# Kernel tuning notes

Hardware: AMD Instinct MI355X
Metric: run time of the kernel (lower is better)

The kernel has to match this reference:

```python
import jax, jax.numpy as jnp
import numpy as np

V, I, H, O = 10000, 64, 128, 128   # vocab, in_size, hidden_size, out_size
T, L = 4096, 64                    # num traces, max trace length


def setup_inputs() -> dict:
    key = jax.random.key(0)
    ks = jax.random.split(key, 18)
    s = 0.05
    n = jax.random.normal
    inp = {
        "emb":   n(ks[0], (V, I)) * s,
        # torch nn.LSTM layer 0: weight_ih [4H, I], weight_hh [4H, H], biases [4H]
        "W_ih1": n(ks[1], (4 * H, I)) * s,
        "W_hh1": n(ks[2], (4 * H, H)) * s,
        "b_ih1": n(ks[3], (4 * H,)) * s,
        "b_hh1": n(ks[4], (4 * H,)) * s,
        # layer 1
        "W_ih2": n(ks[5], (4 * H, H)) * s,
        "W_hh2": n(ks[6], (4 * H, H)) * s,
        "b_ih2": n(ks[7], (4 * H,)) * s,
        "b_hh2": n(ks[8], (4 * H,)) * s,
        # attention MLP: hidden -> 64 -> 1
        "Wp1":   n(ks[9], (64, H)) * s,
        "bp1":   n(ks[10], (64,)) * s,
        "Wp2":   n(ks[11], (1, 64)) * s,
        "bp2":   n(ks[12], (1,)) * s,
        # out_layer
        "W_out": n(ks[13], (O, H)) * s,
        "b_out": n(ks[14], (O,)) * s,
        "traces": jax.random.randint(ks[15], (T, L), 0, V, dtype=jnp.int32),
        "lengths": jnp.maximum(jax.random.randint(ks[16], (T,), 1, L + 1, dtype=jnp.int32), 1),
    }
    return inp


def _lstm_step(x, W_ih, b_ih, b_hh):
    # Single LSTM timestep from zero state (h0=c0=0), per token.
    # Gate order in torch: i, f, g, o. f*c0 = 0 so f is computed-but-unused.
    g = x @ W_ih.T + b_ih + b_hh                      # [T, L, 4H]
    i, f, c_hat, o = jnp.split(g, 4, axis=-1)
    c = jax.nn.sigmoid(i) * jnp.tanh(c_hat)
    return jax.nn.sigmoid(o) * jnp.tanh(c)            # [T, L, H]


def reference(emb, W_ih1, W_hh1, b_ih1, b_hh1, W_ih2, W_hh2, b_ih2, b_hh2,
              Wp1, bp1, Wp2, bp2, W_out, b_out, traces, lengths):
    x = emb[traces]                                   # [T, L, I]
    h1 = _lstm_step(x, W_ih1, b_ih1, b_hh1)           # [T, L, H]
    h2 = _lstm_step(h1, W_ih2, b_ih2, b_hh2)          # [T, L, H]  (hidden_out)
    # SelfAttention over positions within each trace
    energy = (jax.nn.relu(h2 @ Wp1.T + bp1) @ Wp2.T + bp2)[..., 0]  # [T, L]
    mask = jnp.arange(L)[None, :] < lengths[:, None]  # [T, L] valid positions
    energy = jnp.where(mask, energy, -1e30)
    w = jax.nn.softmax(energy, axis=1)                # [T, L]
    trace_emb = jnp.einsum("tlh,tl->th", h2, w)      # [T, H]
    final = trace_emb.sum(axis=0)                     # [H]  (sum over traces)
    return final @ W_out.T + b_out                    # [O]
```

## Files before the change

kernel.cpp:

```cpp
#include <hip/hip_runtime.h>
#include <stdint.h>

typedef unsigned short u16;
typedef __attribute__((ext_vector_type(8))) short short8;
typedef __attribute__((ext_vector_type(4))) float f32x4;
typedef __attribute__((ext_vector_type(4))) unsigned int u32x4;

#define NTRACE 4096
#define TLEN   64
#define ISZ    64
#define HSZ    128
#define NBIN   64
#define VSZ    10000

#define LOG2E     1.44269504088896f
#define TWOLOG2E  2.88539008177793f

__device__ __forceinline__ float bflo(uint32_t u) {
  union { uint32_t i; float f; } v; v.i = u << 16; return v.f;
}
__device__ __forceinline__ float bfhi(uint32_t u) {
  union { uint32_t i; float f; } v; v.i = u & 0xffff0000u; return v.f;
}
__device__ __forceinline__ u16 f2bf(float f) {
  union { float f; uint32_t i; } v; v.f = f;
  uint32_t r = v.i + 0x7fffu + ((v.i >> 16) & 1u);
  return (u16)(r >> 16);
}
__device__ __forceinline__ float fexp2(float x) {
  float r;
  asm("v_exp_f32 %0, %1" : "=v"(r) : "v"(x));
  return r;
}
__device__ __forceinline__ float gate2(float gB, float gE) {
  float E = fexp2(gE);
  float B = fexp2(gB);
  return (E - 1.0f) * __builtin_amdgcn_rcpf((E + 1.0f) * (1.0f + B));
}
__device__ __forceinline__ short8 mk8(uint32_t a, uint32_t b, uint32_t c, uint32_t d) {
  union { short8 s; uint32_t u[4]; } z;
  z.u[0] = a; z.u[1] = b; z.u[2] = c; z.u[3] = d; return z.s;
}
union S8 { short8 s; u16 h[8]; };
__device__ __forceinline__ int perm128(int rr) {
  return ((rr >> 4) & 3) * 32 + ((rr >> 2) & 3) * 8 + ((rr >> 6) & 1) * 4 + (rr & 3);
}

__global__ __launch_bounds__(128, 2) void k_vocab(
    const float* __restrict__ emb,
    const float* __restrict__ W1, const float* __restrict__ W2,
    const float* __restrict__ b_ih1, const float* __restrict__ b_hh1,
    const float* __restrict__ b_ih2, const float* __restrict__ b_hh2,
    const float* __restrict__ Wp1,
    const float* __restrict__ bp1v, const float* __restrict__ wp2v,
    float* __restrict__ Et, u16* __restrict__ H2t,
    float* __restrict__ bins)
{
  __shared__ __align__(16) u16 w1s[384 * 64];
  __shared__ __align__(16) u16 w2s[384 * 128];
  __shared__ float bsh1[512];
  __shared__ float bsh2[512];
  const int tid = threadIdx.x;

  {
    const int i = blockIdx.x * 128 + tid;
    if (i < NBIN * HSZ) bins[i] = 0.f;
  }

  for (int i = tid; i < 3072; i += 128) {
    const int r   = i >> 3;
    const int G3  = r >> 7;
    const int rawG = (G3 == 0) ? 0 : ((G3 == 1) ? 2 : 3);
    const int src = rawG * 128 + perm128(r & 127);
    const float s = (G3 == 1) ? TWOLOG2E : -LOG2E;
    const int c16 = (i & 7) * 8;
    const float* wsrc = W1 + (size_t)src * ISZ + c16;
    uint32_t pkk[4];
#pragma unroll
    for (int k = 0; k < 4; ++k)
      pkk[k] = (uint32_t)f2bf(wsrc[2 * k] * s) |
               ((uint32_t)f2bf(wsrc[2 * k + 1] * s) << 16);
    *(u32x4*)&w1s[r * 64 + (c16 ^ ((r & 7) << 3))] = *(u32x4*)pkk;
  }
  for (int i = tid; i < 6144; i += 128) {
    const int r   = i >> 4;
    const int G3  = r >> 7;
    const int rawG = (G3 == 0) ? 0 : ((G3 == 1) ? 2 : 3);
    const int src = rawG * 128 + perm128(r & 127);
    const float s = (G3 == 1) ? TWOLOG2E : -LOG2E;
    const int c16 = (i & 15) * 8;
    const float* wsrc = W2 + (size_t)src * HSZ + c16;
    uint32_t pkk[4];
#pragma unroll
    for (int k = 0; k < 4; ++k)
      pkk[k] = (uint32_t)f2bf(wsrc[2 * k] * s) |
               ((uint32_t)f2bf(wsrc[2 * k + 1] * s) << 16);
    *(u32x4*)&w2s[r * 128 + (c16 ^ ((r & 15) << 3))] = *(u32x4*)pkk;
  }
  for (int i = tid; i < 512; i += 128) {
    const int G = i >> 7, rr = i & 127;
    const float s = (G == 2) ? TWOLOG2E : -LOG2E;
    const int src = G * 128 + perm128(rr);
    bsh1[i] = (b_ih1[src] + b_hh1[src]) * s;
    bsh2[i] = (b_ih2[src] + b_hh2[src]) * s;
  }
  __syncthreads();

  const int lane = tid & 63;
  const int col  = lane & 15;
  const int q    = lane >> 4;
  const int sw1  = (col & 7) << 3;
  const int sw2  = col << 3;
  const int wbase = (blockIdx.x * 2 + (tid >> 6)) * 32;
  const f32x4 z = {0.f, 0.f, 0.f, 0.f};

  short8 xf[2][2];
#pragma unroll
  for (int g = 0; g < 2; ++g) {
    const int id = wbase + g * 16 + col;
    const int idc = (id < VSZ) ? id : 0;
    const float* xr = emb + (size_t)idc * ISZ + q * 8;
#pragma unroll
    for (int ks = 0; ks < 2; ++ks) {
      S8 v;
#pragma unroll
      for (int k = 0; k < 8; ++k) v.h[k] = f2bf(xr[ks * 32 + k]);
      xf[g][ks] = v.s;
    }
  }

  uint32_t pk[2][8][2];
#pragma unroll
  for (int mt = 0; mt < 8; ++mt) {
    f32x4 aI[2], aC[2], aO[2];
#pragma unroll
    for (int g = 0; g < 2; ++g) { aI[g] = z; aC[g] = z; aO[g] = z; }
#pragma unroll
    for (int ks = 0; ks < 2; ++ks) {
      const int off = ((ks * 32 + q * 8) ^ sw1);
      short8 fI = *(const short8*)&w1s[(mt * 16 + col) * ISZ + off];
      short8 fC = *(const short8*)&w1s[(128 + mt * 16 + col) * ISZ + off];
      short8 fO = *(const short8*)&w1s[(256 + mt * 16 + col) * ISZ + off];
#pragma unroll
      for (int g = 0; g < 2; ++g) {
        aI[g] = __builtin_amdgcn_mfma_f32_16x16x32_bf16(fI, xf[g][ks], aI[g], 0, 0, 0);
        aC[g] = __builtin_amdgcn_mfma_f32_16x16x32_bf16(fC, xf[g][ks], aC[g], 0, 0, 0);
        aO[g] = __builtin_amdgcn_mfma_f32_16x16x32_bf16(fO, xf[g][ks], aO[g], 0, 0, 0);
      }
    }
    float bI[4], bC[4], bO[4];
#pragma unroll
    for (int r = 0; r < 4; ++r) {
      const int h = mt * 16 + q * 4 + r;
      bI[r] = bsh1[h]; bC[r] = bsh1[256 + h]; bO[r] = bsh1[384 + h];
    }
#pragma unroll
    for (int g = 0; g < 2; ++g) {
      u16 hv[4];
#pragma unroll
      for (int r = 0; r < 4; ++r) {
        float c = gate2(aI[g][r] + bI[r], aC[g][r] + bC[r]);
        hv[r] = f2bf(gate2(aO[g][r] + bO[r], TWOLOG2E * c));
      }
      pk[g][mt][0] = (uint32_t)hv[0] | ((uint32_t)hv[1] << 16);
      pk[g][mt][1] = (uint32_t)hv[2] | ((uint32_t)hv[3] << 16);
    }
  }

  short8 hf[2][4];
#pragma unroll
  for (int g = 0; g < 2; ++g)
#pragma unroll
    for (int ks = 0; ks < 4; ++ks)
      hf[g][ks] = mk8(pk[g][ks][0], pk[g][ks][1], pk[g][ks + 4][0], pk[g][ks + 4][1]);

  uint32_t pk2[2][8][2];
#pragma unroll
  for (int mt = 0; mt < 8; ++mt) {
    f32x4 aI[2], aC[2], aO[2];
#pragma unroll
    for (int g = 0; g < 2; ++g) { aI[g] = z; aC[g] = z; aO[g] = z; }
#pragma unroll
    for (int ks = 0; ks < 4; ++ks) {
      const int off = ((ks * 32 + q * 8) ^ sw2);
      short8 fI = *(const short8*)&w2s[(mt * 16 + col) * HSZ + off];
      short8 fC = *(const short8*)&w2s[(128 + mt * 16 + col) * HSZ + off];
      short8 fO = *(const short8*)&w2s[(256 + mt * 16 + col) * HSZ + off];
#pragma unroll
      for (int g = 0; g < 2; ++g) {
        aI[g] = __builtin_amdgcn_mfma_f32_16x16x32_bf16(fI, hf[g][ks], aI[g], 0, 0, 0);
        aC[g] = __builtin_amdgcn_mfma_f32_16x16x32_bf16(fC, hf[g][ks], aC[g], 0, 0, 0);
        aO[g] = __builtin_amdgcn_mfma_f32_16x16x32_bf16(fO, hf[g][ks], aO[g], 0, 0, 0);
      }
    }
    float bI[4], bC[4], bO[4];
#pragma unroll
    for (int r = 0; r < 4; ++r) {
      const int h = mt * 16 + q * 4 + r;
      bI[r] = bsh2[h]; bC[r] = bsh2[256 + h]; bO[r] = bsh2[384 + h];
    }
#pragma unroll
    for (int g = 0; g < 2; ++g) {
      u16 hv[4];
#pragma unroll
      for (int r = 0; r < 4; ++r) {
        float c = gate2(aI[g][r] + bI[r], aC[g][r] + bC[r]);
        hv[r] = f2bf(gate2(aO[g][r] + bO[r], TWOLOG2E * c));
      }
      pk2[g][mt][0] = (uint32_t)hv[0] | ((uint32_t)hv[1] << 16);
      pk2[g][mt][1] = (uint32_t)hv[2] | ((uint32_t)hv[3] << 16);
    }
  }

  short8 hf2[2][4];
#pragma unroll
  for (int g = 0; g < 2; ++g)
#pragma unroll
    for (int ks = 0; ks < 4; ++ks)
      hf2[g][ks] = mk8(pk2[g][ks][0], pk2[g][ks][1], pk2[g][ks + 4][0], pk2[g][ks + 4][1]);

  float ep[2];
#pragma unroll
  for (int g = 0; g < 2; ++g) ep[g] = 0.f;
#pragma unroll
  for (int mt = 0; mt < 4; ++mt) {
    f32x4 acc[2];
#pragma unroll
    for (int g = 0; g < 2; ++g) acc[g] = z;
#pragma unroll
    for (int ks = 0; ks < 4; ++ks) {
      const float* wr = Wp1 + (size_t)(mt * 16 + col) * HSZ + ks * 32 + q * 8;
      S8 v;
#pragma unroll
      for (int k = 0; k < 8; ++k) v.h[k] = f2bf(wr[k]);
      const short8 fA = v.s;
#pragma unroll
      for (int g = 0; g < 2; ++g)
        acc[g] = __builtin_amdgcn_mfma_f32_16x16x32_bf16(fA, hf2[g][ks], acc[g], 0, 0, 0);
    }
#pragma unroll
    for (int r = 0; r < 4; ++r) {
      const int hp = mt * 16 + q * 4 + r;
      const float b1 = bp1v[hp];
      const float w2 = wp2v[hp];
#pragma unroll
      for (int g = 0; g < 2; ++g)
        ep[g] += fmaxf(acc[g][r] + b1, 0.f) * w2;
    }
  }
#pragma unroll
  for (int g = 0; g < 2; ++g) {
    ep[g] += __shfl_xor(ep[g], 16);
    ep[g] += __shfl_xor(ep[g], 32);
  }

#pragma unroll
  for (int g = 0; g < 2; ++g) {
    const int id = wbase + g * 16 + col;
    if (id < VSZ) {
      if (q == 0) Et[id] = ep[g];
#pragma unroll
      for (int ks = 0; ks < 4; ++ks)
        *(short8*)&H2t[(size_t)id * HSZ + ks * 32 + q * 8] = hf2[g][ks];
    }
  }
}

__global__ __launch_bounds__(256) void k_attn(
    const float* __restrict__ Et, const u16* __restrict__ H2t,
    const int* __restrict__ traces, const int* __restrict__ lengths,
    float* __restrict__ bins)
{
  const int wv   = threadIdx.x >> 6;
  const int lane = threadIdx.x & 63;
  const int t    = blockIdx.x * 4 + wv;
  const int len  = lengths[t];
  const int tok  = traces[t * TLEN + lane];
  const bool valid = lane < len;

  float e = valid ? Et[tok] : -3.0e38f;
  float m = e;
#pragma unroll
  for (int off = 1; off < 64; off <<= 1) m = fmaxf(m, __shfl_xor(m, off));
  float w = valid ? __expf(e - m) : 0.f;
  float s = w;
#pragma unroll
  for (int off = 1; off < 64; off <<= 1) s += __shfl_xor(s, off);
  const float wl = w * __builtin_amdgcn_rcpf(s);

  const int hc = lane * 2;
  float a0 = 0.f, a1 = 0.f;
  for (int l = 0; l < len; ++l) {
    const float wb = __shfl(wl, l);
    const int   tb = __shfl(tok, l);
    const uint32_t hv = *(const uint32_t*)&H2t[(size_t)tb * HSZ + hc];
    a0 += wb * bflo(hv);
    a1 += wb * bfhi(hv);
  }
  float* bin = bins + (size_t)(t & (NBIN - 1)) * HSZ;
  atomicAdd(&bin[hc], a0);
  atomicAdd(&bin[hc + 1], a1);
}

__global__ __launch_bounds__(128) void k_out(
    const float* __restrict__ bins, const float* __restrict__ W_out,
    const float* __restrict__ b_out, float* __restrict__ out)
{
  const int o = threadIdx.x;
  __shared__ float fs[HSZ];
  float s = 0.f;
#pragma unroll 4
  for (int b = 0; b < NBIN; ++b) s += bins[b * HSZ + o];
  fs[o] = s;
  __syncthreads();
  float acc = b_out[o];
  const float* wr = W_out + (size_t)o * HSZ;
#pragma unroll
  for (int h = 0; h < HSZ; ++h) acc += wr[h] * fs[h];
  out[o] = acc;
}

extern "C" void kernel_launch(void* const* d_in, const int* in_sizes, int n_in,
                              void* d_out, int out_size, void* d_ws, size_t ws_size,
                              hipStream_t stream)
{
  const float* emb   = (const float*)d_in[0];
  const float* W_ih1 = (const float*)d_in[1];
  const float* b_ih1 = (const float*)d_in[3];
  const float* b_hh1 = (const float*)d_in[4];
  const float* W_ih2 = (const float*)d_in[5];
  const float* b_ih2 = (const float*)d_in[7];
  const float* b_hh2 = (const float*)d_in[8];
  const float* Wp1   = (const float*)d_in[9];
  const float* bp1   = (const float*)d_in[10];
  const float* Wp2   = (const float*)d_in[11];
  const float* bp2   = (const float*)d_in[12];
  const float* W_out = (const float*)d_in[13];
  const float* b_out = (const float*)d_in[14];
  const int* traces  = (const int*)d_in[15];
  const int* lengths = (const int*)d_in[16];
  (void)bp2;

  char* ws = (char*)d_ws;
  float* Et   = (float*)(ws);
  u16*   H2t  = (u16*)(ws + 40960);
  float* bins = (float*)(ws + 2662400);

  k_vocab<<<160, 128, 0, stream>>>(emb, W_ih1, W_ih2, b_ih1, b_hh1,
                                   b_ih2, b_hh2, Wp1, bp1, Wp2,
                                   Et, H2t, bins);
  k_attn<<<NTRACE / 4, 256, 0, stream>>>(Et, H2t, traces, lengths, bins);
  k_out<<<1, 128, 0, stream>>>(bins, W_out, b_out, (float*)d_out);
}
```

Measured before the change: 153.7 us.

## Split weight conversion into prep kernel and widen vocab blocks to 512 threads

Adds a k_prep kernel that converts and swizzles the LSTM and attention weights to bf16 once, writing them to workspace along with pre-scaled biases and zeroed bins. k_vocab then copies the prepacked weights straight into shared memory. It now runs 80 blocks of 512 threads, with each wave handling 16 vocab rows instead of 32. The aim is to stop every block from redoing the fp32-to-bf16 conversion and to spread the per-block weight load across more waves. The cost is one extra kernel launch and less MFMA operand reuse per wave, and the biases and Wp1 are now read from global memory rather than shared memory.

```diff
diff --git a/kernel.cpp b/kernel.cpp
--- a/kernel.cpp
+++ b/kernel.cpp
@@ -46,64 +46,73 @@
   return ((rr >> 4) & 3) * 32 + ((rr >> 2) & 3) * 8 + ((rr >> 6) & 1) * 4 + (rr & 3);
 }
 
-__global__ __launch_bounds__(128, 2) void k_vocab(
-    const float* __restrict__ emb,
+__global__ __launch_bounds__(256) void k_prep(
     const float* __restrict__ W1, const float* __restrict__ W2,
+    const float* __restrict__ Wp1,
     const float* __restrict__ b_ih1, const float* __restrict__ b_hh1,
     const float* __restrict__ b_ih2, const float* __restrict__ b_hh2,
-    const float* __restrict__ Wp1,
-    const float* __restrict__ bp1v, const float* __restrict__ wp2v,
-    float* __restrict__ Et, u16* __restrict__ H2t,
+    u16* __restrict__ w1c, u16* __restrict__ w2c, u16* __restrict__ wp1b,
+    float* __restrict__ bs1, float* __restrict__ bs2,
     float* __restrict__ bins)
 {
-  __shared__ __align__(16) u16 w1s[384 * 64];
-  __shared__ __align__(16) u16 w2s[384 * 128];
-  __shared__ float bsh1[512];
-  __shared__ float bsh2[512];
-  const int tid = threadIdx.x;
-
-  {
-    const int i = blockIdx.x * 128 + tid;
-    if (i < NBIN * HSZ) bins[i] = 0.f;
-  }
-
-  for (int i = tid; i < 3072; i += 128) {
-    const int r   = i >> 3;
-    const int G3  = r >> 7;
+  const int i = blockIdx.x * 256 + threadIdx.x;
+  if (i < 3072) {
+    const int r    = i >> 3;
+    const int G3   = r >> 7;
     const int rawG = (G3 == 0) ? 0 : ((G3 == 1) ? 2 : 3);
-    const int src = rawG * 128 + perm128(r & 127);
-    const float s = (G3 == 1) ? TWOLOG2E : -LOG2E;
-    const int c16 = (i & 7) * 8;
+    const int src  = rawG * 128 + perm128(r & 127);
+    const float s  = (G3 == 1) ? TWOLOG2E : -LOG2E;
+    const int c16  = (i & 7) * 8;
     const float* wsrc = W1 + (size_t)src * ISZ + c16;
     uint32_t pkk[4];
 #pragma unroll
     for (int k = 0; k < 4; ++k)
       pkk[k] = (uint32_t)f2bf(wsrc[2 * k] * s) |
                ((uint32_t)f2bf(wsrc[2 * k + 1] * s) << 16);
-    *(u32x4*)&w1s[r * 64 + (c16 ^ ((r & 7) << 3))] = *(u32x4*)pkk;
-  }
-  for (int i = tid; i < 6144; i += 128) {
-    const int r   = i >> 4;
-    const int G3  = r >> 7;
+    *(u32x4*)&w1c[r * 64 + (c16 ^ ((r & 7) << 3))] = *(u32x4*)pkk;
+  }
+  if (i < 6144) {
+    const int r    = i >> 4;
+    const int G3   = r >> 7;
     const int rawG = (G3 == 0) ? 0 : ((G3 == 1) ? 2 : 3);
-    const int src = rawG * 128 + perm128(r & 127);
-    const float s = (G3 == 1) ? TWOLOG2E : -LOG2E;
-    const int c16 = (i & 15) * 8;
+    const int src  = rawG * 128 + perm128(r & 127);
+    const float s  = (G3 == 1) ? TWOLOG2E : -LOG2E;
+    const int c16  = (i & 15) * 8;
     const float* wsrc = W2 + (size_t)src * HSZ + c16;
     uint32_t pkk[4];
 #pragma unroll
     for (int k = 0; k < 4; ++k)
       pkk[k] = (uint32_t)f2bf(wsrc[2 * k] * s) |
                ((uint32_t)f2bf(wsrc[2 * k + 1] * s) << 16);
-    *(u32x4*)&w2s[r * 128 + (c16 ^ ((r & 15) << 3))] = *(u32x4*)pkk;
-  }
-  for (int i = tid; i < 512; i += 128) {
+    *(u32x4*)&w2c[r * 128 + (c16 ^ ((r & 15) << 3))] = *(u32x4*)pkk;
+  }
+  if (i < 64 * 128) wp1b[i] = f2bf(Wp1[i]);
+  if (i < 512) {
     const int G = i >> 7, rr = i & 127;
     const float s = (G == 2) ? TWOLOG2E : -LOG2E;
     const int src = G * 128 + perm128(rr);
-    bsh1[i] = (b_ih1[src] + b_hh1[src]) * s;
-    bsh2[i] = (b_ih2[src] + b_hh2[src]) * s;
-  }
+    bs1[i] = (b_ih1[src] + b_hh1[src]) * s;
+    bs2[i] = (b_ih2[src] + b_hh2[src]) * s;
+  }
+  if (i < NBIN * HSZ) bins[i] = 0.f;
+}
+
+__global__ __launch_bounds__(512) void k_vocab(
+    const float* __restrict__ emb,
+    const u16* __restrict__ w1c, const u16* __restrict__ w2c,
+    const float* __restrict__ bs1, const float* __restrict__ bs2,
+    const u16* __restrict__ wp1b,
+    const float* __restrict__ bp1v, const float* __restrict__ wp2v,
+    float* __restrict__ Et, u16* __restrict__ H2t)
+{
+  __shared__ __align__(16) u16 w1s[384 * 64];
+  __shared__ __align__(16) u16 w2s[384 * 128];
+  const int tid = threadIdx.x;
+
+  for (int i = tid; i < 3072; i += 512)
+    ((u32x4*)w1s)[i] = ((const u32x4*)w1c)[i];
+  for (int i = tid; i < 6144; i += 512)
+    ((u32x4*)w2s)[i] = ((const u32x4*)w2c)[i];
   __syncthreads();
 
   const int lane = tid & 63;
@@ -111,158 +120,105 @@
   const int q    = lane >> 4;
   const int sw1  = (col & 7) << 3;
   const int sw2  = col << 3;
-  const int wbase = (blockIdx.x * 2 + (tid >> 6)) * 32;
+  const int id   = (blockIdx.x * 8 + (tid >> 6)) * 16 + col;
+  const int idc  = (id < VSZ) ? id : 0;
   const f32x4 z = {0.f, 0.f, 0.f, 0.f};
 
-  short8 xf[2][2];
-#pragma unroll
-  for (int g = 0; g < 2; ++g) {
-    const int id = wbase + g * 16 + col;
-    const int idc = (id < VSZ) ? id : 0;
+  short8 xf[2];
+  {
     const float* xr = emb + (size_t)idc * ISZ + q * 8;
 #pragma unroll
     for (int ks = 0; ks < 2; ++ks) {
       S8 v;
 #pragma unroll
       for (int k = 0; k < 8; ++k) v.h[k] = f2bf(xr[ks * 32 + k]);
-      xf[g][ks] = v.s;
-    }
-  }
-
-  uint32_t pk[2][8][2];
+      xf[ks] = v.s;
+    }
+  }
+
+  uint32_t pk[8][2];
 #pragma unroll
   for (int mt = 0; mt < 8; ++mt) {
-    f32x4 aI[2], aC[2], aO[2];
-#pragma unroll
-    for (int g = 0; g < 2; ++g) { aI[g] = z; aC[g] = z; aO[g] = z; }
+    f32x4 aI = z, aC = z, aO = z;
 #pragma unroll
     for (int ks = 0; ks < 2; ++ks) {
       const int off = ((ks * 32 + q * 8) ^ sw1);
       short8 fI = *(const short8*)&w1s[(mt * 16 + col) * ISZ + off];
       short8 fC = *(const short8*)&w1s[(128 + mt * 16 + col) * ISZ + off];
       short8 fO = *(const short8*)&w1s[(256 + mt * 16 + col) * ISZ + off];
-#pragma unroll
-      for (int g = 0; g < 2; ++g) {
-        aI[g] = __builtin_amdgcn_mfma_f32_16x16x32_bf16(fI, xf[g][ks], aI[g], 0, 0, 0);
-        aC[g] = __builtin_amdgcn_mfma_f32_16x16x32_bf16(fC, xf[g][ks], aC[g], 0, 0, 0);
-        aO[g] = __builtin_amdgcn_mfma_f32_16x16x32_bf16(fO, xf[g][ks], aO[g], 0, 0, 0);
-      }
-    }
-    float bI[4], bC[4], bO[4];
+      aI = __builtin_amdgcn_mfma_f32_16x16x32_bf16(fI, xf[ks], aI, 0, 0, 0);
+      aC = __builtin_amdgcn_mfma_f32_16x16x32_bf16(fC, xf[ks], aC, 0, 0, 0);
+      aO = __builtin_amdgcn_mfma_f32_16x16x32_bf16(fO, xf[ks], aO, 0, 0, 0);
+    }
+    u16 hv[4];
 #pragma unroll
     for (int r = 0; r < 4; ++r) {
       const int h = mt * 16 + q * 4 + r;
-      bI[r] = bsh1[h]; bC[r] = bsh1[256 + h]; bO[r] = bsh1[384 + h];
-    }
-#pragma unroll
-    for (int g = 0; g < 2; ++g) {
-      u16 hv[4];
-#pragma unroll
-      for (int r = 0; r < 4; ++r) {
-        float c = gate2(aI[g][r] + bI[r], aC[g][r] + bC[r]);
-        hv[r] = f2bf(gate2(aO[g][r] + bO[r], TWOLOG2E * c));
-      }
-      pk[g][mt][0] = (uint32_t)hv[0] | ((uint32_t)hv[1] << 16);
-      pk[g][mt][1] = (uint32_t)hv[2] | ((uint32_t)hv[3] << 16);
-    }
-  }
-
-  short8 hf[2][4];
-#pragma unroll
-  for (int g = 0; g < 2; ++g)
-#pragma unroll
-    for (int ks = 0; ks < 4; ++ks)
-      hf[g][ks] = mk8(pk[g][ks][0], pk[g][ks][1], pk[g][ks + 4][0], pk[g][ks + 4][1]);
-
-  uint32_t pk2[2][8][2];
+      float c = gate2(aI[r] + bs1[h], aC[r] + bs1[256 + h]);
+      hv[r] = f2bf(gate2(aO[r] + bs1[384 + h], TWOLOG2E * c));
+    }
+    pk[mt][0] = (uint32_t)hv[0] | ((uint32_t)hv[1] << 16);
+    pk[mt][1] = (uint32_t)hv[2] | ((uint32_t)hv[3] << 16);
+  }
+
+  short8 hf[4];
+#pragma unroll
+  for (int ks = 0; ks < 4; ++ks)
+    hf[ks] = mk8(pk[ks][0], pk[ks][1], pk[ks + 4][0], pk[ks + 4][1]);
+
+  uint32_t pk2[8][2];
 #pragma unroll
   for (int mt = 0; mt < 8; ++mt) {
-    f32x4 aI[2], aC[2], aO[2];
-#pragma unroll
-    for (int g = 0; g < 2; ++g) { aI[g] = z; aC[g] = z; aO[g] = z; }
+    f32x4 aI = z, aC = z, aO = z;
 #pragma unroll
     for (int ks = 0; ks < 4; ++ks) {
       const int off = ((ks * 32 + q * 8) ^ sw2);
       short8 fI = *(const short8*)&w2s[(mt * 16 + col) * HSZ + off];
       short8 fC = *(const short8*)&w2s[(128 + mt * 16 + col) * HSZ + off];
       short8 fO = *(const short8*)&w2s[(256 + mt * 16 + col) * HSZ + off];
-#pragma unroll
-      for (int g = 0; g < 2; ++g) {
-        aI[g] = __builtin_amdgcn_mfma_f32_16x16x32_bf16(fI, hf[g][ks], aI[g], 0, 0, 0);
-        aC[g] = __builtin_amdgcn_mfma_f32_16x16x32_bf16(fC, hf[g][ks], aC[g], 0, 0, 0);
-        aO[g] = __builtin_amdgcn_mfma_f32_16x16x32_bf16(fO, hf[g][ks], aO[g], 0, 0, 0);
-      }
-    }
-    float bI[4], bC[4], bO[4];
+      aI = __builtin_amdgcn_mfma_f32_16x16x32_bf16(fI, hf[ks], aI, 0, 0, 0);
+      aC = __builtin_amdgcn_mfma_f32_16x16x32_bf16(fC, hf[ks], aC, 0, 0, 0);
+      aO = __builtin_amdgcn_mfma_f32_16x16x32_bf16(fO, hf[ks], aO, 0, 0, 0);
+    }
+    u16 hv[4];
 #pragma unroll
     for (int r = 0; r < 4; ++r) {
       const int h = mt * 16 + q * 4 + r;
-      bI[r] = bsh2[h]; bC[r] = bsh2[256 + h]; bO[r] = bsh2[384 + h];
-    }
-#pragma unroll
-    for (int g = 0; g < 2; ++g) {
-      u16 hv[4];
-#pragma unroll
-      for (int r = 0; r < 4; ++r) {
-        float c = gate2(aI[g][r] + bI[r], aC[g][r] + bC[r]);
-        hv[r] = f2bf(gate2(aO[g][r] + bO[r], TWOLOG2E * c));
-      }
-      pk2[g][mt][0] = (uint32_t)hv[0] | ((uint32_t)hv[1] << 16);
-      pk2[g][mt][1] = (uint32_t)hv[2] | ((uint32_t)hv[3] << 16);
-    }
-  }
-
-  short8 hf2[2][4];
-#pragma unroll
-  for (int g = 0; g < 2; ++g)
-#pragma unroll
-    for (int ks = 0; ks < 4; ++ks)
-      hf2[g][ks] = mk8(pk2[g][ks][0], pk2[g][ks][1], pk2[g][ks + 4][0], pk2[g][ks + 4][1]);
-
-  float ep[2];
-#pragma unroll
-  for (int g = 0; g < 2; ++g) ep[g] = 0.f;
+      float c = gate2(aI[r] + bs2[h], aC[r] + bs2[256 + h]);
+      hv[r] = f2bf(gate2(aO[r] + bs2[384 + h], TWOLOG2E * c));
+    }
+    pk2[mt][0] = (uint32_t)hv[0] | ((uint32_t)hv[1] << 16);
+    pk2[mt][1] = (uint32_t)hv[2] | ((uint32_t)hv[3] << 16);
+  }
+
+  short8 hf2[4];
+#pragma unroll
+  for (int ks = 0; ks < 4; ++ks)
+    hf2[ks] = mk8(pk2[ks][0], pk2[ks][1], pk2[ks + 4][0], pk2[ks + 4][1]);
+
+  float ep = 0.f;
 #pragma unroll
   for (int mt = 0; mt < 4; ++mt) {
-    f32x4 acc[2];
-#pragma unroll
-    for (int g = 0; g < 2; ++g) acc[g] = z;
+    f32x4 acc = z;
 #pragma unroll
     for (int ks = 0; ks < 4; ++ks) {
-      const float* wr = Wp1 + (size_t)(mt * 16 + col) * HSZ + ks * 32 + q * 8;
-      S8 v;
-#pragma unroll
-      for (int k = 0; k < 8; ++k) v.h[k] = f2bf(wr[k]);
-      const short8 fA = v.s;
-#pragma unroll
-      for (int g = 0; g < 2; ++g)
-        acc[g] = __builtin_amdgcn_mfma_f32_16x16x32_bf16(fA, hf2[g][ks], acc[g], 0, 0, 0);
+      short8 fA = *(const short8*)(wp1b + (size_t)(mt * 16 + col) * HSZ + ks * 32 + q * 8);
+      acc = __builtin_amdgcn_mfma_f32_16x16x32_bf16(fA, hf2[ks], acc, 0, 0, 0);
     }
 #pragma unroll
     for (int r = 0; r < 4; ++r) {
       const int hp = mt * 16 + q * 4 + r;
-      const float b1 = bp1v[hp];
-      const float w2 = wp2v[hp];
-#pragma unroll
-      for (int g = 0; g < 2; ++g)
-        ep[g] += fmaxf(acc[g][r] + b1, 0.f) * w2;
-    }
-  }
-#pragma unroll
-  for (int g = 0; g < 2; ++g) {
-    ep[g] += __shfl_xor(ep[g], 16);
-    ep[g] += __shfl_xor(ep[g], 32);
-  }
-
-#pragma unroll
-  for (int g = 0; g < 2; ++g) {
-    const int id = wbase + g * 16 + col;
-    if (id < VSZ) {
-      if (q == 0) Et[id] = ep[g];
-#pragma unroll
-      for (int ks = 0; ks < 4; ++ks)
-        *(short8*)&H2t[(size_t)id * HSZ + ks * 32 + q * 8] = hf2[g][ks];
-    }
+      ep += fmaxf(acc[r] + bp1v[hp], 0.f) * wp2v[hp];
+    }
+  }
+  ep += __shfl_xor(ep, 16);
+  ep += __shfl_xor(ep, 32);
+
+  if (id < VSZ) {
+    if (q == 0) Et[id] = ep;
+#pragma unroll
+    for (int ks = 0; ks < 4; ++ks)
+      *(short8*)&H2t[(size_t)id * HSZ + ks * 32 + q * 8] = hf2[ks];
   }
 }
 
@@ -345,10 +301,17 @@
   float* Et   = (float*)(ws);
   u16*   H2t  = (u16*)(ws + 40960);
   float* bins = (float*)(ws + 2662400);
-
-  k_vocab<<<160, 128, 0, stream>>>(emb, W_ih1, W_ih2, b_ih1, b_hh1,
-                                   b_ih2, b_hh2, Wp1, bp1, Wp2,
-                                   Et, H2t, bins);
+  u16*   w1c  = (u16*)(ws + 2695168);
+  u16*   w2c  = (u16*)(ws + 2744320);
+  u16*   wp1b = (u16*)(ws + 2842624);
+  float* bs1  = (float*)(ws + 2859008);
+  float* bs2  = (float*)(ws + 2861056);
+
+  k_prep<<<32, 256, 0, stream>>>(W_ih1, W_ih2, Wp1, b_ih1, b_hh1,
+                                 b_ih2, b_hh2, w1c, w2c, wp1b,
+                                 bs1, bs2, bins);
+  k_vocab<<<80, 512, 0, stream>>>(emb, w1c, w2c, bs1, bs2, wp1b,
+                                  bp1, Wp2, Et, H2t);
   k_attn<<<NTRACE / 4, 256, 0, stream>>>(Et, H2t, traces, lengths, bins);
   k_out<<<1, 128, 0, stream>>>(bins, W_out, b_out, (float*)d_out);
 }
```

Result: faster. 138.3 us (-10.0%).
